# Optimization experiments

Hardware: AMD Instinct MI355X
Metric: run time of the kernel (lower is better)

Reference implementation:

```python
import jax, jax.numpy as jnp
import numpy as np
from jax import lax

STEPS = 16
CHANNELS = 64
HIDDEN = 1024
LENGTH = 2048
BATCH = 32
EPS = 1e-5

def setup_inputs() -> dict:
    key = jax.random.key(0)
    ks = jax.random.split(key, 8)
    x = jax.random.normal(ks[0], (BATCH, CHANNELS, LENGTH), dtype=jnp.float32)
    # Conv1d params (PyTorch layout OIH for weights)
    s1 = 1.0 / np.sqrt(CHANNELS * 3)
    s2 = 1.0 / np.sqrt(HIDDEN)
    w1 = jax.random.uniform(ks[1], (HIDDEN, CHANNELS, 3), jnp.float32, -s1, s1)
    b1 = jax.random.uniform(ks[2], (HIDDEN,), jnp.float32, -s1, s1)
    w2 = jax.random.uniform(ks[3], (HIDDEN, HIDDEN), jnp.float32, -s2, s2)
    b2 = jax.random.uniform(ks[4], (HIDDEN,), jnp.float32, -s2, s2)
    w3 = jax.random.uniform(ks[5], (CHANNELS, HIDDEN), jnp.float32, -s2, s2)
    b3 = jax.random.uniform(ks[6], (CHANNELS,), jnp.float32, -s2, s2)
    # LayerNorm([channels, length]) elementwise affine
    gamma = jnp.ones((CHANNELS, LENGTH), dtype=jnp.float32)
    beta = jnp.zeros((CHANNELS, LENGTH), dtype=jnp.float32)
    return {"x": x, "w1": w1, "b1": b1, "w2": w2, "b2": b2,
            "w3": w3, "b3": b3, "gamma": gamma, "beta": beta}

def reference(x, w1, b1, w2, b2, w3, b3, gamma, beta):
    # Eval-mode forward: dropout is identity, no noise injection.
    def step(x, _):
        # conv1: k=3, pad=1  -> [B, HIDDEN, L]
        h = lax.conv_general_dilated(
            x, w1, window_strides=(1,), padding=[(1, 1)],
            dimension_numbers=("NCH", "OIH", "NCH"))
        h = jax.nn.relu(h + b1[None, :, None])
        # conv2: 1x1 (pointwise) -> GEMM over channel dim
        h = jnp.einsum("oh,bhl->bol", w2, h) + b2[None, :, None]
        h = jax.nn.relu(h)
        # conv3: 1x1 back to channels
        h = jnp.einsum("ch,bhl->bcl", w3, h) + b3[None, :, None]
        x = x + h  # residual
        # LayerNorm over [channels, length] per sample
        mu = jnp.mean(x, axis=(1, 2), keepdims=True)
        var = jnp.var(x, axis=(1, 2), keepdims=True)
        x = (x - mu) * lax.rsqrt(var + EPS) * gamma[None] + beta[None]
        return x, None

    x, _ = lax.scan(step, x, None, length=STEPS)
    return x
```

## Files before the change

### kernel.cpp

```cpp
#include <hip/hip_runtime.h>
#include <stdint.h>

#define L_LEN 2048
#define LP (L_LEN + 2)
#define CH 64
#define HID 1024
#define NSTEP 16
#define NB 32
#define EPS_F 1e-5f

typedef __bf16 bf16x8 __attribute__((ext_vector_type(8)));
typedef float f32x4 __attribute__((ext_vector_type(4)));

__device__ __forceinline__ float u16f(unsigned short u){
  unsigned int x = ((unsigned int)u) << 16;
  return __builtin_bit_cast(float, x);
}
__device__ __forceinline__ unsigned short f2u(float f){
  unsigned int x = __builtin_bit_cast(unsigned int, f);
  unsigned int r = x + 0x7FFFu + ((x >> 16) & 1u);
  return (unsigned short)(r >> 16);
}

__device__ __forceinline__ void gload16(const unsigned short* g, const unsigned short* l){
  __builtin_amdgcn_global_load_lds(
      (const __attribute__((address_space(1))) unsigned int*)g,
      (__attribute__((address_space(3))) unsigned int*)l, 16, 0, 0);
}

__global__ void flag_k(const unsigned int* __restrict__ gamma, int* __restrict__ flag){
  *flag = (gamma[0] == 0x3F803F80u) ? 1 : 0;
}

__global__ __launch_bounds__(256)
void conv_k(const void* __restrict__ src, unsigned short* __restrict__ dst, int n,
            const int* __restrict__ flagp){
  int fl = *flagp;
  for (int i = blockIdx.x * 256 + threadIdx.x; i < n; i += gridDim.x * 256){
    dst[i] = fl ? ((const unsigned short*)src)[i] : f2u(((const float*)src)[i]);
  }
}

__global__ __launch_bounds__(256)
void packw1_k(const void* __restrict__ w1, unsigned short* __restrict__ w1p,
              const int* __restrict__ flagp){
  int idx = blockIdx.x * 256 + threadIdx.x;
  int o = idx / 192;
  int r = idx - o * 192;
  int t = r >> 6;
  int c = r & 63;
  int sidx = (o * 64 + c) * 3 + t;
  w1p[idx] = (*flagp) ? ((const unsigned short*)w1)[sidx]
                      : f2u(((const float*)w1)[sidx]);
}

__global__ __launch_bounds__(256)
void pad_k(unsigned short* __restrict__ xbfT){
  int i = blockIdx.x * 256 + threadIdx.x;
  int s = i >> 7;
  int r = i & 127;
  size_t row = (r >> 6) ? (size_t)(LP - 1) : 0;
  xbfT[((size_t)s * LP + row) * CH + (r & 63)] = 0;
}

__global__ __launch_bounds__(256)
void init_k(const void* __restrict__ xin, float* __restrict__ xf,
            unsigned short* __restrict__ xbfT, const int* __restrict__ flagp){
  int t = blockIdx.x * 256 + threadIdx.x;
  size_t i0 = (size_t)t * 4;
  float4 f;
  if (*flagp){
    ushort4 v = *reinterpret_cast<const ushort4*>(&((const unsigned short*)xin)[i0]);
    f = make_float4(u16f(v.x), u16f(v.y), u16f(v.z), u16f(v.w));
  } else {
    f = *reinterpret_cast<const float4*>(&((const float*)xin)[i0]);
  }
  *reinterpret_cast<float4*>(&xf[i0]) = f;
  int s = (int)(i0 >> 17);
  int r = (int)(i0 & 131071);
  int c = r >> 11;
  int l = r & 2047;
  unsigned short* d = &xbfT[((size_t)s * LP + l + 1) * CH + c];
  d[0]      = f2u(f.x);
  d[CH]     = f2u(f.y);
  d[2 * CH] = f2u(f.z);
  d[3 * CH] = f2u(f.w);
}

template<int QM>
__device__ __forceinline__ void ld_a(const unsigned short* lb, int wm, int lane,
                                     bf16x8 (&af)[4][2]){
  #pragma unroll
  for (int i = 0; i < 4; i++)
    #pragma unroll
    for (int kk = 0; kk < 2; kk++){
      int r  = wm * 128 + QM * 64 + i * 16 + (lane & 15);
      int cb = kk * 4 + (lane >> 4);
      af[i][kk] = *reinterpret_cast<const bf16x8*>(lb + r * 64 + ((cb ^ (r & 7)) << 3));
    }
}
template<int QN>
__device__ __forceinline__ void ld_b(const unsigned short* lb, int wn, int lane,
                                     bf16x8 (&bfr)[2][2][2]){
  #pragma unroll
  for (int j = 0; j < 2; j++)
    #pragma unroll
    for (int kk = 0; kk < 2; kk++){
      int r  = wn * 64 + QN * 32 + j * 16 + (lane & 15);
      int cb = kk * 4 + (lane >> 4);
      bfr[QN][j][kk] = *reinterpret_cast<const bf16x8*>(lb + 16384 + r * 64 + ((cb ^ (r & 7)) << 3));
    }
}
template<int QM, int QN>
__device__ __forceinline__ void mfma_q(f32x4 (&acc)[8][4], bf16x8 (&af)[4][2],
                                       bf16x8 (&bfr)[2][2][2]){
  #pragma unroll
  for (int i = 0; i < 4; i++)
    #pragma unroll
    for (int j = 0; j < 2; j++)
      #pragma unroll
      for (int kk = 0; kk < 2; kk++)
        acc[QM * 4 + i][QN * 2 + j] = __builtin_amdgcn_mfma_f32_16x16x32_bf16(
            af[i][kk], bfr[QN][j][kk], acc[QM * 4 + i][QN * 2 + j], 0, 0, 0);
}

#define SYNC_MID() do { __builtin_amdgcn_s_barrier(); \
  asm volatile("s_waitcnt lgkmcnt(0)" ::: "memory"); \
  __builtin_amdgcn_sched_barrier(0); \
  __builtin_amdgcn_s_setprio(1); } while(0)
#define SYNC_END0() do { __builtin_amdgcn_s_setprio(0); \
  __builtin_amdgcn_s_barrier(); } while(0)
#define SYNC_ENDV() do { __builtin_amdgcn_s_setprio(0); \
  asm volatile("s_waitcnt vmcnt(4)" ::: "memory"); \
  __builtin_amdgcn_s_barrier(); } while(0)

__global__ __launch_bounds__(512, 2)
void gemm8_k(const unsigned short* __restrict__ A,
             const unsigned short* __restrict__ Bx,
             const unsigned short* __restrict__ bias,
             unsigned short* __restrict__ OutB)
{
  __shared__ __align__(16) unsigned short lds[65536];
  const int tid  = threadIdx.x;
  const int lane = tid & 63;
  const int wave = tid >> 6;
  const int wm   = wave >> 2;
  const int wn   = wave & 3;

  const int nwg = gridDim.x;
  const int bid = blockIdx.x;
  const int qq = nwg >> 3, rr = nwg & 7;
  const int xcd = bid & 7, loc = bid >> 3;
  const int wg = (xcd < rr) ? (xcd * (qq + 1) + loc)
                            : (rr * (qq + 1) + (xcd - rr) * qq + loc);
  const int bx = wg & 3;
  const int t_ = wg >> 2;
  const int by = t_ & 7;
  const int bb = t_ >> 3;
  const int m0 = bx * 256;
  const int n0 = by * 256;

  const unsigned short* Bb = Bx + (size_t)bb * L_LEN * HID;

  f32x4 acc[8][4];
  #pragma unroll
  for (int i = 0; i < 8; i++)
    #pragma unroll
    for (int j = 0; j < 4; j++)
      #pragma unroll
      for (int v = 0; v < 4; v++) acc[i][j][v] = 0.f;

  bf16x8 af[4][2];
  bf16x8 bfr[2][2][2];

  auto STAGE_A = [&](int t, int buf, int half){
    #pragma unroll
    for (int li = 0; li < 2; li++){
      int q = li * 512 + tid;
      int row = q >> 3, cc = q & 7;
      int scc = cc ^ (row & 7);
      gload16(&A[(size_t)(m0 + half * 128 + row) * HID + t * 64 + scc * 8],
              lds + buf * 32768 + half * 8192 + (li * 512 + wave * 64) * 8);
    }
  };
  auto STAGE_B = [&](int t, int buf, int half){
    #pragma unroll
    for (int li = 0; li < 2; li++){
      int q = li * 512 + tid;
      int row = q >> 3, cc = q & 7;
      int scc = cc ^ (row & 7);
      gload16(&Bb[(size_t)(n0 + half * 128 + row) * HID + t * 64 + scc * 8],
              lds + buf * 32768 + 16384 + half * 8192 + (li * 512 + wave * 64) * 8);
    }
  };

  const unsigned short* L0 = lds;
  const unsigned short* L1 = lds + 32768;

  STAGE_B(0, 0, 0); STAGE_B(0, 0, 1);
  STAGE_A(0, 0, 0); STAGE_A(0, 0, 1);
  STAGE_B(1, 1, 0); STAGE_B(1, 1, 1);
  asm volatile("s_waitcnt vmcnt(4)" ::: "memory");
  __builtin_amdgcn_s_barrier();

  for (int it = 0; it < 8; it++){
    int t1 = 2 * it + 1;
    int t2 = (2 * it + 2 < 16) ? 2 * it + 2 : 15;
    int t3 = (2 * it + 3 < 16) ? 2 * it + 3 : 15;
    ld_a<0>(L0, wm, lane, af); ld_b<0>(L0, wn, lane, bfr);
    STAGE_A(t1, 1, 0);
    SYNC_MID(); mfma_q<0, 0>(acc, af, bfr); SYNC_END0();
    ld_b<1>(L0, wn, lane, bfr);
    STAGE_A(t1, 1, 1);
    SYNC_MID(); mfma_q<0, 1>(acc, af, bfr); SYNC_END0();
    ld_a<1>(L0, wm, lane, af);
    STAGE_B(t2, 0, 0);
    SYNC_MID(); mfma_q<1, 0>(acc, af, bfr); SYNC_END0();
    STAGE_B(t2, 0, 1);
    SYNC_MID(); mfma_q<1, 1>(acc, af, bfr); SYNC_ENDV();
    ld_a<0>(L1, wm, lane, af); ld_b<0>(L1, wn, lane, bfr);
    STAGE_A(t2, 0, 0);
    SYNC_MID(); mfma_q<0, 0>(acc, af, bfr); SYNC_END0();
    ld_b<1>(L1, wn, lane, bfr);
    STAGE_A(t2, 0, 1);
    SYNC_MID(); mfma_q<0, 1>(acc, af, bfr); SYNC_END0();
    ld_a<1>(L1, wm, lane, af);
    STAGE_B(t3, 1, 0);
    SYNC_MID(); mfma_q<1, 0>(acc, af, bfr); SYNC_END0();
    STAGE_B(t3, 1, 1);
    SYNC_MID(); mfma_q<1, 1>(acc, af, bfr); SYNC_ENDV();
  }

  #pragma unroll
  for (int i = 0; i < 8; i++){
    int mb_ = m0 + wm * 128 + i * 16 + ((lane >> 4) << 2);
    float bv0 = u16f(bias[mb_ + 0]), bv1 = u16f(bias[mb_ + 1]);
    float bv2 = u16f(bias[mb_ + 2]), bv3 = u16f(bias[mb_ + 3]);
    #pragma unroll
    for (int j = 0; j < 4; j++){
      int n = n0 + wn * 64 + j * 16 + (lane & 15);
      ushort4 pk;
      pk.x = f2u(fmaxf(acc[i][j][0] + bv0, 0.f));
      pk.y = f2u(fmaxf(acc[i][j][1] + bv1, 0.f));
      pk.z = f2u(fmaxf(acc[i][j][2] + bv2, 0.f));
      pk.w = f2u(fmaxf(acc[i][j][3] + bv3, 0.f));
      *reinterpret_cast<ushort4*>(&OutB[((size_t)bb * L_LEN + n) * HID + mb_]) = pk;
    }
  }
}

__global__ __launch_bounds__(512, 4)
void c1_k(const unsigned short* __restrict__ A,
          const unsigned short* __restrict__ Bx,
          const unsigned short* __restrict__ bias,
          unsigned short* __restrict__ OutB)
{
  __shared__ __align__(16) unsigned short lA1[128 * 192];
  __shared__ __align__(16) unsigned short lB1[136 * 64];
  const int tid  = threadIdx.x;
  const int lane = tid & 63;
  const int wave = tid >> 6;
  const int wm   = wave >> 2;
  const int wn   = wave & 3;

  const int nwg = gridDim.x;
  const int bid = blockIdx.x;
  const int qq = nwg >> 3, rr = nwg & 7;
  const int xcd = bid & 7, loc = bid >> 3;
  const int wg = (xcd < rr) ? (xcd * (qq + 1) + loc)
                            : (rr * (qq + 1) + (xcd - rr) * qq + loc);
  const int bx = wg & 7;
  const int t_ = wg >> 3;
  const int by = t_ & 15;
  const int bb = t_ >> 4;
  const int m0 = bx * 128;
  const int n0 = by * 128;

  #pragma unroll
  for (int p = 0; p < 6; p++){
    int q = p * 512 + tid;
    int row = q / 24, cc = q % 24;
    int scc = cc ^ (row & 7);
    gload16(&A[(size_t)(m0 + row) * 192 + scc * 8], &lA1[(p * 512 + wave * 64) * 8]);
  }
  #pragma unroll
  for (int p = 0; p < 2; p++){
    int q = p * 512 + tid;
    int row = q >> 3, cc = q & 7;
    int scc = cc ^ (row & 7);
    int srow = n0 + row; if (srow > LP - 1) srow = LP - 1;
    gload16(&Bx[((size_t)bb * LP + srow) * CH + scc * 8], &lB1[(p * 512 + wave * 64) * 8]);
  }
  if (wave == 0){
    int q = 1024 + lane;
    int row = q >> 3, cc = q & 7;
    int scc = cc ^ (row & 7);
    int srow = n0 + row; if (srow > LP - 1) srow = LP - 1;
    gload16(&Bx[((size_t)bb * LP + srow) * CH + scc * 8], &lB1[1024 * 8]);
  }
  asm volatile("s_waitcnt vmcnt(0)" ::: "memory");
  __builtin_amdgcn_s_barrier();

  f32x4 acc[4][2];
  #pragma unroll
  for (int i = 0; i < 4; i++)
    #pragma unroll
    for (int j = 0; j < 2; j++)
      #pragma unroll
      for (int v = 0; v < 4; v++) acc[i][j][v] = 0.f;

  #pragma unroll
  for (int t = 0; t < 3; t++){
    #pragma unroll
    for (int kk = 0; kk < 2; kk++){
      bf16x8 af[4], bf[2];
      int cb  = t * 8 + kk * 4 + (lane >> 4);
      int cb2 = kk * 4 + (lane >> 4);
      #pragma unroll
      for (int i = 0; i < 4; i++){
        int r = wm * 64 + i * 16 + (lane & 15);
        af[i] = *reinterpret_cast<const bf16x8*>(&lA1[r * 192 + ((cb ^ (r & 7)) << 3)]);
      }
      #pragma unroll
      for (int j = 0; j < 2; j++){
        int r = wn * 32 + j * 16 + (lane & 15) + t;
        bf[j] = *reinterpret_cast<const bf16x8*>(&lB1[r * 64 + ((cb2 ^ (r & 7)) << 3)]);
      }
      #pragma unroll
      for (int i = 0; i < 4; i++)
        #pragma unroll
        for (int j = 0; j < 2; j++)
          acc[i][j] = __builtin_amdgcn_mfma_f32_16x16x32_bf16(af[i], bf[j], acc[i][j], 0, 0, 0);
    }
  }

  #pragma unroll
  for (int i = 0; i < 4; i++){
    int mb_ = m0 + wm * 64 + i * 16 + ((lane >> 4) << 2);
    float bv0 = u16f(bias[mb_ + 0]), bv1 = u16f(bias[mb_ + 1]);
    float bv2 = u16f(bias[mb_ + 2]), bv3 = u16f(bias[mb_ + 3]);
    #pragma unroll
    for (int j = 0; j < 2; j++){
      int n = n0 + wn * 32 + j * 16 + (lane & 15);
      ushort4 pk;
      pk.x = f2u(fmaxf(acc[i][j][0] + bv0, 0.f));
      pk.y = f2u(fmaxf(acc[i][j][1] + bv1, 0.f));
      pk.z = f2u(fmaxf(acc[i][j][2] + bv2, 0.f));
      pk.w = f2u(fmaxf(acc[i][j][3] + bv3, 0.f));
      *reinterpret_cast<ushort4*>(&OutB[((size_t)bb * L_LEN + n) * HID + mb_]) = pk;
    }
  }
}

__global__ __launch_bounds__(256)
void c3_k(const unsigned short* __restrict__ A,
          const unsigned short* __restrict__ Bx,
          const unsigned short* __restrict__ bias,
          float* __restrict__ OutX,
          float2* __restrict__ part)
{
  __shared__ __align__(16) unsigned short lA2[2][64 * 64];
  __shared__ __align__(16) unsigned short lB2[2][128 * 64];
  __shared__ float2 wsum[4];
  const int tid  = threadIdx.x;
  const int lane = tid & 63;
  const int wave = tid >> 6;
  const int wn   = wave;

  const int nwg = gridDim.x;
  const int bid = blockIdx.x;
  const int qq = nwg >> 3, rr = nwg & 7;
  const int xcd = bid & 7, loc = bid >> 3;
  const int wg = (xcd < rr) ? (xcd * (qq + 1) + loc)
                            : (rr * (qq + 1) + (xcd - rr) * qq + loc);
  const int by = wg & 15;
  const int bb = wg >> 4;
  const int n0 = by * 128;

  auto STAGE = [&](int t, int buf){
    #pragma unroll
    for (int i = 0; i < 2; i++){
      int q = i * 256 + tid;
      int row = q >> 3, cc = q & 7;
      int scc = cc ^ (row & 7);
      gload16(&A[(size_t)row * HID + t * 64 + scc * 8], &lA2[buf][(i * 256 + wave * 64) * 8]);
    }
    #pragma unroll
    for (int i = 0; i < 4; i++){
      int q = i * 256 + tid;
      int row = q >> 3, cc = q & 7;
      int scc = cc ^ (row & 7);
      gload16(&Bx[((size_t)bb * L_LEN + n0 + row) * HID + t * 64 + scc * 8],
              &lB2[buf][(i * 256 + wave * 64) * 8]);
    }
  };

  f32x4 acc[4][2];
  #pragma unroll
  for (int i = 0; i < 4; i++)
    #pragma unroll
    for (int j = 0; j < 2; j++)
      #pragma unroll
      for (int v = 0; v < 4; v++) acc[i][j][v] = 0.f;

  STAGE(0, 0);
  __syncthreads();
  for (int t = 0; t < 16; t++){
    int cur = t & 1;
    if (t < 15) STAGE(t + 1, cur ^ 1);
    #pragma unroll
    for (int kk = 0; kk < 2; kk++){
      bf16x8 af[4], bf[2];
      int cb = kk * 4 + (lane >> 4);
      #pragma unroll
      for (int i = 0; i < 4; i++){
        int r = i * 16 + (lane & 15);
        af[i] = *reinterpret_cast<const bf16x8*>(&lA2[cur][r * 64 + ((cb ^ (r & 7)) << 3)]);
      }
      #pragma unroll
      for (int j = 0; j < 2; j++){
        int r = wn * 32 + j * 16 + (lane & 15);
        bf[j] = *reinterpret_cast<const bf16x8*>(&lB2[cur][r * 64 + ((cb ^ (r & 7)) << 3)]);
      }
      #pragma unroll
      for (int i = 0; i < 4; i++)
        #pragma unroll
        for (int j = 0; j < 2; j++)
          acc[i][j] = __builtin_amdgcn_mfma_f32_16x16x32_bf16(af[i], bf[j], acc[i][j], 0, 0, 0);
    }
    __syncthreads();
  }

  float lsum = 0.f, lsq = 0.f;
  #pragma unroll
  for (int i = 0; i < 4; i++){
    int c0 = i * 16 + ((lane >> 4) << 2);
    float bv[4] = { u16f(bias[c0 + 0]), u16f(bias[c0 + 1]),
                    u16f(bias[c0 + 2]), u16f(bias[c0 + 3]) };
    #pragma unroll
    for (int j = 0; j < 2; j++){
      int n = n0 + wn * 32 + j * 16 + (lane & 15);
      #pragma unroll
      for (int v = 0; v < 4; v++){
        float* p = &OutX[((size_t)bb * CH + c0 + v) * L_LEN + n];
        float val = *p + acc[i][j][v] + bv[v];
        *p = val;
        lsum += val; lsq += val * val;
      }
    }
  }
  #pragma unroll
  for (int off = 32; off > 0; off >>= 1){
    lsum += __shfl_xor(lsum, off);
    lsq  += __shfl_xor(lsq, off);
  }
  if (lane == 0) wsum[wave] = make_float2(lsum, lsq);
  __syncthreads();
  if (tid == 0){
    float s0 = 0.f, s1 = 0.f;
    #pragma unroll
    for (int i = 0; i < 4; i++){ s0 += wsum[i].x; s1 += wsum[i].y; }
    part[bb * 16 + by] = make_float2(s0, s1);
  }
}

__global__ __launch_bounds__(256)
void ln_k(float* __restrict__ x, const float2* __restrict__ part,
          const unsigned short* __restrict__ gamma, const unsigned short* __restrict__ beta,
          unsigned short* __restrict__ xbfT, void* __restrict__ dout,
          const int* __restrict__ flagp, int last)
{
  int s = blockIdx.x;
  float sum = 0.f, sq = 0.f;
  #pragma unroll
  for (int i = 0; i < 16; i++){ float2 p = part[s * 16 + i]; sum += p.x; sq += p.y; }
  const float inv = 1.f / (float)(CH * L_LEN);
  float mean = sum * inv;
  float var  = fmaxf(sq * inv - mean * mean, 0.f);
  float rstd = rsqrtf(var + EPS_F);

  int i0 = (blockIdx.y * 256 + threadIdx.x) * 4;
  size_t g = (size_t)s * (CH * L_LEN) + i0;
  float4 v = *reinterpret_cast<const float4*>(&x[g]);
  ushort4 gm = *reinterpret_cast<const ushort4*>(&gamma[i0]);
  ushort4 bt = *reinterpret_cast<const ushort4*>(&beta[i0]);
  float o0 = (v.x - mean) * rstd * u16f(gm.x) + u16f(bt.x);
  float o1 = (v.y - mean) * rstd * u16f(gm.y) + u16f(bt.y);
  float o2 = (v.z - mean) * rstd * u16f(gm.z) + u16f(bt.z);
  float o3 = (v.w - mean) * rstd * u16f(gm.w) + u16f(bt.w);
  *reinterpret_cast<float4*>(&x[g]) = make_float4(o0, o1, o2, o3);
  if (last){
    if (*flagp){
      ushort4 pk = { f2u(o0), f2u(o1), f2u(o2), f2u(o3) };
      *reinterpret_cast<ushort4*>(&((unsigned short*)dout)[g]) = pk;
    } else {
      *reinterpret_cast<float4*>(&((float*)dout)[g]) = make_float4(o0, o1, o2, o3);
    }
  } else {
    int c = i0 >> 11;
    int l = i0 & 2047;
    unsigned short* d = &xbfT[((size_t)s * LP + l + 1) * CH + c];
    d[0]      = f2u(o0);
    d[CH]     = f2u(o1);
    d[2 * CH] = f2u(o2);
    d[3 * CH] = f2u(o3);
  }
}

extern "C" void kernel_launch(void* const* d_in, const int* in_sizes, int n_in,
                              void* d_out, int out_size, void* d_ws, size_t ws_size,
                              hipStream_t stream)
{
  const void* xin   = d_in[0];
  const void* w1    = d_in[1];
  const void* b1    = d_in[2];
  const void* w2    = d_in[3];
  const void* b2    = d_in[4];
  const void* w3    = d_in[5];
  const void* b3    = d_in[6];
  const void* gamma = d_in[7];
  const void* beta  = d_in[8];

  char* ws = (char*)d_ws;
  size_t off = 0;
  auto alloc = [&](size_t bytes)->char*{
    char* p = ws + off;
    off = (off + bytes + 255) & ~(size_t)255;
    return p;
  };

  float*          x_f32 = (float*)alloc((size_t)NB * CH * L_LEN * 4);
  unsigned short* xbfT  = (unsigned short*)alloc((size_t)NB * LP * CH * 2);
  unsigned short* w1p   = (unsigned short*)alloc((size_t)HID * 192 * 2);
  unsigned short* w2c   = (unsigned short*)alloc((size_t)HID * HID * 2);
  unsigned short* w3c   = (unsigned short*)alloc((size_t)CH * HID * 2);
  unsigned short* b1c   = (unsigned short*)alloc(HID * 2);
  unsigned short* b2c   = (unsigned short*)alloc(HID * 2);
  unsigned short* b3c   = (unsigned short*)alloc(CH * 2);
  unsigned short* gmc   = (unsigned short*)alloc((size_t)CH * L_LEN * 2);
  unsigned short* btc   = (unsigned short*)alloc((size_t)CH * L_LEN * 2);
  float2*         part  = (float2*)alloc(NB * 16 * sizeof(float2));
  int*            flag  = (int*)alloc(256);

  size_t rem = (ws_size > off) ? ws_size - off : 0;
  size_t per_b = (size_t)L_LEN * HID * 2 * 2;
  int bc = NB;
  while (bc > 1 && (size_t)bc * per_b > rem) bc >>= 1;
  unsigned short* h1 = (unsigned short*)(ws + off);
  unsigned short* h2 = h1 + (size_t)bc * L_LEN * HID;

  flag_k<<<1, 1, 0, stream>>>((const unsigned int*)gamma, flag);
  conv_k<<<4096, 256, 0, stream>>>(w2, w2c, HID * HID, flag);
  conv_k<<<256, 256, 0, stream>>>(w3, w3c, CH * HID, flag);
  conv_k<<<4, 256, 0, stream>>>(b1, b1c, HID, flag);
  conv_k<<<4, 256, 0, stream>>>(b2, b2c, HID, flag);
  conv_k<<<1, 256, 0, stream>>>(b3, b3c, CH, flag);
  conv_k<<<512, 256, 0, stream>>>(gamma, gmc, CH * L_LEN, flag);
  conv_k<<<512, 256, 0, stream>>>(beta, btc, CH * L_LEN, flag);
  packw1_k<<<768, 256, 0, stream>>>(w1, w1p, flag);
  pad_k<<<16, 256, 0, stream>>>(xbfT);
  init_k<<<4096, 256, 0, stream>>>(xin, x_f32, xbfT, flag);

  for (int step = 0; step < NSTEP; ++step){
    for (int cb = 0; cb < NB; cb += bc){
      c1_k<<<dim3(8 * 16 * bc), 512, 0, stream>>>(
          w1p, xbfT + (size_t)cb * LP * CH, b1c, h1);
      gemm8_k<<<dim3(4 * 8 * bc), 512, 0, stream>>>(w2c, h1, b2c, h2);
      c3_k<<<dim3(16 * bc), 256, 0, stream>>>(
          w3c, h2, b3c, x_f32 + (size_t)cb * CH * L_LEN, part + (size_t)cb * 16);
    }
    ln_k<<<dim3(NB, 128), 256, 0, stream>>>(x_f32, part, gmc, btc, xbfT, d_out, flag,
                                            step == NSTEP - 1 ? 1 : 0);
  }
}
```

Measured before the change: 4.154 ms.

## Fuse conv3 GEMM into conv2 epilogue with split-K partials and reduce kernel

The conv2 GEMM kernel no longer writes the full HIDDEN-wide activation h2 to global memory. It stages its 256-row ReLU output tile in LDS and multiplies it by the matching slice of W3 right there, producing a bf16 partial conv3 result per M-block (split-K over 4 blocks). A new lightweight res_k sums the 4 partials, adds bias and the residual, and computes the LayerNorm partial statistics. This removes the large h2 write and re-read plus the separate conv3 GEMM. In exchange it adds bf16 rounding of the partials, extra epilogue work and W3 global loads inside the GEMM kernel.

```diff
diff --git a/kernel.cpp b/kernel.cpp
--- a/kernel.cpp
+++ b/kernel.cpp
@@ -10,6 +10,7 @@
 #define EPS_F 1e-5f
 
 typedef __bf16 bf16x8 __attribute__((ext_vector_type(8)));
+typedef unsigned short u16x8 __attribute__((ext_vector_type(8)));
 typedef float f32x4 __attribute__((ext_vector_type(4)));
 
 __device__ __forceinline__ float u16f(unsigned short u){
@@ -138,7 +139,8 @@
 void gemm8_k(const unsigned short* __restrict__ A,
              const unsigned short* __restrict__ Bx,
              const unsigned short* __restrict__ bias,
-             unsigned short* __restrict__ OutB)
+             const unsigned short* __restrict__ W3,
+             unsigned short* __restrict__ P3)
 {
   __shared__ __align__(16) unsigned short lds[65536];
   const int tid  = threadIdx.x;
@@ -231,20 +233,70 @@
     SYNC_MID(); mfma_q<1, 1>(acc, af, bfr); SYNC_ENDV();
   }
 
+  asm volatile("s_waitcnt vmcnt(0)" ::: "memory");
+  __builtin_amdgcn_s_barrier();
+
+  unsigned short* T = lds;
   #pragma unroll
   for (int i = 0; i < 8; i++){
-    int mb_ = m0 + wm * 128 + i * 16 + ((lane >> 4) << 2);
-    float bv0 = u16f(bias[mb_ + 0]), bv1 = u16f(bias[mb_ + 1]);
-    float bv2 = u16f(bias[mb_ + 2]), bv3 = u16f(bias[mb_ + 3]);
+    int o0 = wm * 128 + i * 16 + ((lane >> 4) << 2);
+    int og = m0 + o0;
+    float bv0 = u16f(bias[og + 0]), bv1 = u16f(bias[og + 1]);
+    float bv2 = u16f(bias[og + 2]), bv3 = u16f(bias[og + 3]);
+    int co = o0 >> 3;
     #pragma unroll
     for (int j = 0; j < 4; j++){
-      int n = n0 + wn * 64 + j * 16 + (lane & 15);
+      int n = wn * 64 + j * 16 + (lane & 15);
       ushort4 pk;
       pk.x = f2u(fmaxf(acc[i][j][0] + bv0, 0.f));
       pk.y = f2u(fmaxf(acc[i][j][1] + bv1, 0.f));
       pk.z = f2u(fmaxf(acc[i][j][2] + bv2, 0.f));
       pk.w = f2u(fmaxf(acc[i][j][3] + bv3, 0.f));
-      *reinterpret_cast<ushort4*>(&OutB[((size_t)bb * L_LEN + n) * HID + mb_]) = pk;
+      *reinterpret_cast<ushort4*>(&T[n * 256 + (((co ^ (n & 7)) << 3) | (o0 & 7))]) = pk;
+    }
+  }
+  __builtin_amdgcn_s_barrier();
+
+  f32x4 a3[2][4];
+  #pragma unroll
+  for (int nt = 0; nt < 2; nt++)
+    #pragma unroll
+    for (int ct = 0; ct < 4; ct++)
+      #pragma unroll
+      for (int v = 0; v < 4; v++) a3[nt][ct][v] = 0.f;
+
+  #pragma unroll
+  for (int kk = 0; kk < 8; kk++){
+    bf16x8 wf[4];
+    #pragma unroll
+    for (int ct = 0; ct < 4; ct++){
+      int c = ct * 16 + (lane & 15);
+      wf[ct] = *reinterpret_cast<const bf16x8*>(
+          &W3[(size_t)c * HID + m0 + kk * 32 + ((lane >> 4) << 3)]);
+    }
+    #pragma unroll
+    for (int nt = 0; nt < 2; nt++){
+      int n = (wave * 2 + nt) * 16 + (lane & 15);
+      int cb = kk * 4 + (lane >> 4);
+      bf16x8 tf = *reinterpret_cast<const bf16x8*>(&T[n * 256 + ((cb ^ (n & 7)) << 3)]);
+      #pragma unroll
+      for (int ct = 0; ct < 4; ct++)
+        a3[nt][ct] = __builtin_amdgcn_mfma_f32_16x16x32_bf16(wf[ct], tf, a3[nt][ct], 0, 0, 0);
+    }
+  }
+
+  #pragma unroll
+  for (int nt = 0; nt < 2; nt++){
+    int n = n0 + (wave * 2 + nt) * 16 + (lane & 15);
+    #pragma unroll
+    for (int ct = 0; ct < 4; ct++){
+      int c0 = ct * 16 + ((lane >> 4) << 2);
+      ushort4 pk;
+      pk.x = f2u(a3[nt][ct][0]);
+      pk.y = f2u(a3[nt][ct][1]);
+      pk.z = f2u(a3[nt][ct][2]);
+      pk.w = f2u(a3[nt][ct][3]);
+      *reinterpret_cast<ushort4*>(&P3[((size_t)(bb * 4 + bx) * L_LEN + n) * CH + c0]) = pk;
     }
   }
 }
@@ -353,114 +405,66 @@
 }
 
 __global__ __launch_bounds__(256)
-void c3_k(const unsigned short* __restrict__ A,
-          const unsigned short* __restrict__ Bx,
-          const unsigned short* __restrict__ bias,
-          float* __restrict__ OutX,
-          float2* __restrict__ part)
+void res_k(const unsigned short* __restrict__ P3,
+           const unsigned short* __restrict__ b3,
+           float* __restrict__ OutX,
+           float2* __restrict__ part)
 {
-  __shared__ __align__(16) unsigned short lA2[2][64 * 64];
-  __shared__ __align__(16) unsigned short lB2[2][128 * 64];
+  __shared__ float accl[64][129];
   __shared__ float2 wsum[4];
-  const int tid  = threadIdx.x;
-  const int lane = tid & 63;
-  const int wave = tid >> 6;
-  const int wn   = wave;
-
-  const int nwg = gridDim.x;
-  const int bid = blockIdx.x;
-  const int qq = nwg >> 3, rr = nwg & 7;
-  const int xcd = bid & 7, loc = bid >> 3;
-  const int wg = (xcd < rr) ? (xcd * (qq + 1) + loc)
-                            : (rr * (qq + 1) + (xcd - rr) * qq + loc);
-  const int by = wg & 15;
-  const int bb = wg >> 4;
-  const int n0 = by * 128;
-
-  auto STAGE = [&](int t, int buf){
-    #pragma unroll
-    for (int i = 0; i < 2; i++){
-      int q = i * 256 + tid;
-      int row = q >> 3, cc = q & 7;
-      int scc = cc ^ (row & 7);
-      gload16(&A[(size_t)row * HID + t * 64 + scc * 8], &lA2[buf][(i * 256 + wave * 64) * 8]);
-    }
-    #pragma unroll
-    for (int i = 0; i < 4; i++){
-      int q = i * 256 + tid;
-      int row = q >> 3, cc = q & 7;
-      int scc = cc ^ (row & 7);
-      gload16(&Bx[((size_t)bb * L_LEN + n0 + row) * HID + t * 64 + scc * 8],
-              &lB2[buf][(i * 256 + wave * 64) * 8]);
-    }
-  };
-
-  f32x4 acc[4][2];
-  #pragma unroll
-  for (int i = 0; i < 4; i++)
-    #pragma unroll
-    for (int j = 0; j < 2; j++)
-      #pragma unroll
-      for (int v = 0; v < 4; v++) acc[i][j][v] = 0.f;
-
-  STAGE(0, 0);
+  const int tid = threadIdx.x;
+  const int nb = blockIdx.x & 15;
+  const int bb = blockIdx.x >> 4;
+  const int n0 = nb * 128;
+
+  #pragma unroll
+  for (int p = 0; p < 4; p++){
+    int n  = p * 32 + (tid >> 3);
+    int c0 = (tid & 7) * 8;
+    float v[8];
+    #pragma unroll
+    for (int j = 0; j < 8; j++) v[j] = 0.f;
+    #pragma unroll
+    for (int bx = 0; bx < 4; bx++){
+      u16x8 r = *reinterpret_cast<const u16x8*>(
+          &P3[((size_t)(bb * 4 + bx) * L_LEN + n0 + n) * CH + c0]);
+      #pragma unroll
+      for (int j = 0; j < 8; j++) v[j] += u16f(r[j]);
+    }
+    #pragma unroll
+    for (int j = 0; j < 8; j++) accl[c0 + j][n] = v[j];
+  }
   __syncthreads();
-  for (int t = 0; t < 16; t++){
-    int cur = t & 1;
-    if (t < 15) STAGE(t + 1, cur ^ 1);
-    #pragma unroll
-    for (int kk = 0; kk < 2; kk++){
-      bf16x8 af[4], bf[2];
-      int cb = kk * 4 + (lane >> 4);
-      #pragma unroll
-      for (int i = 0; i < 4; i++){
-        int r = i * 16 + (lane & 15);
-        af[i] = *reinterpret_cast<const bf16x8*>(&lA2[cur][r * 64 + ((cb ^ (r & 7)) << 3)]);
-      }
-      #pragma unroll
-      for (int j = 0; j < 2; j++){
-        int r = wn * 32 + j * 16 + (lane & 15);
-        bf[j] = *reinterpret_cast<const bf16x8*>(&lB2[cur][r * 64 + ((cb ^ (r & 7)) << 3)]);
-      }
-      #pragma unroll
-      for (int i = 0; i < 4; i++)
-        #pragma unroll
-        for (int j = 0; j < 2; j++)
-          acc[i][j] = __builtin_amdgcn_mfma_f32_16x16x32_bf16(af[i], bf[j], acc[i][j], 0, 0, 0);
-    }
-    __syncthreads();
-  }
 
   float lsum = 0.f, lsq = 0.f;
   #pragma unroll
-  for (int i = 0; i < 4; i++){
-    int c0 = i * 16 + ((lane >> 4) << 2);
-    float bv[4] = { u16f(bias[c0 + 0]), u16f(bias[c0 + 1]),
-                    u16f(bias[c0 + 2]), u16f(bias[c0 + 3]) };
-    #pragma unroll
-    for (int j = 0; j < 2; j++){
-      int n = n0 + wn * 32 + j * 16 + (lane & 15);
-      #pragma unroll
-      for (int v = 0; v < 4; v++){
-        float* p = &OutX[((size_t)bb * CH + c0 + v) * L_LEN + n];
-        float val = *p + acc[i][j][v] + bv[v];
-        *p = val;
-        lsum += val; lsq += val * val;
-      }
-    }
+  for (int q = 0; q < 8; q++){
+    int idx = q * 256 + tid;
+    int c = idx >> 5;
+    int n4 = (idx & 31) * 4;
+    float bv = u16f(b3[c]);
+    float* px = &OutX[((size_t)bb * CH + c) * L_LEN + n0 + n4];
+    float4 xv = *reinterpret_cast<const float4*>(px);
+    float o0 = xv.x + accl[c][n4 + 0] + bv;
+    float o1 = xv.y + accl[c][n4 + 1] + bv;
+    float o2 = xv.z + accl[c][n4 + 2] + bv;
+    float o3 = xv.w + accl[c][n4 + 3] + bv;
+    *reinterpret_cast<float4*>(px) = make_float4(o0, o1, o2, o3);
+    lsum += o0 + o1 + o2 + o3;
+    lsq  += o0 * o0 + o1 * o1 + o2 * o2 + o3 * o3;
   }
   #pragma unroll
   for (int off = 32; off > 0; off >>= 1){
     lsum += __shfl_xor(lsum, off);
     lsq  += __shfl_xor(lsq, off);
   }
-  if (lane == 0) wsum[wave] = make_float2(lsum, lsq);
+  if ((tid & 63) == 0) wsum[tid >> 6] = make_float2(lsum, lsq);
   __syncthreads();
   if (tid == 0){
     float s0 = 0.f, s1 = 0.f;
     #pragma unroll
     for (int i = 0; i < 4; i++){ s0 += wsum[i].x; s1 += wsum[i].y; }
-    part[bb * 16 + by] = make_float2(s0, s1);
+    part[bb * 16 + nb] = make_float2(s0, s1);
   }
 }
 
@@ -543,11 +547,11 @@
   int*            flag  = (int*)alloc(256);
 
   size_t rem = (ws_size > off) ? ws_size - off : 0;
-  size_t per_b = (size_t)L_LEN * HID * 2 * 2;
+  size_t per_b = (size_t)L_LEN * HID * 2 + (size_t)4 * L_LEN * CH * 2;
   int bc = NB;
   while (bc > 1 && (size_t)bc * per_b > rem) bc >>= 1;
   unsigned short* h1 = (unsigned short*)(ws + off);
-  unsigned short* h2 = h1 + (size_t)bc * L_LEN * HID;
+  unsigned short* p3 = h1 + (size_t)bc * L_LEN * HID;
 
   flag_k<<<1, 1, 0, stream>>>((const unsigned int*)gamma, flag);
   conv_k<<<4096, 256, 0, stream>>>(w2, w2c, HID * HID, flag);
@@ -565,9 +569,9 @@
     for (int cb = 0; cb < NB; cb += bc){
       c1_k<<<dim3(8 * 16 * bc), 512, 0, stream>>>(
           w1p, xbfT + (size_t)cb * LP * CH, b1c, h1);
-      gemm8_k<<<dim3(4 * 8 * bc), 512, 0, stream>>>(w2c, h1, b2c, h2);
-      c3_k<<<dim3(16 * bc), 256, 0, stream>>>(
-          w3c, h2, b3c, x_f32 + (size_t)cb * CH * L_LEN, part + (size_t)cb * 16);
+      gemm8_k<<<dim3(4 * 8 * bc), 512, 0, stream>>>(w2c, h1, b2c, w3c, p3);
+      res_k<<<dim3(16 * bc), 256, 0, stream>>>(
+          p3, b3c, x_f32 + (size_t)cb * CH * L_LEN, part + (size_t)cb * 16);
     }
     ln_k<<<dim3(NB, 128), 256, 0, stream>>>(x_f32, part, gmc, btc, xbfT, d_out, flag,
                                             step == NSTEP - 1 ? 1 : 0);
```

Result: faster. 3.735 ms, median of 2 (-10.1%).
